# Kernel optimization log

Hardware: AMD Instinct MI355X
Metric: run time of the kernel (lower is better)

The kernel has to match this reference:

```python
import jax, jax.numpy as jnp
import numpy as np

N_NODES = 100000
N_EDGES = 1600000
IN_FEATS = 128
HEADS = 4
OUT_FEATS = 32
NEG_SLOPE = 0.2


def setup_inputs() -> dict:
    key = jax.random.key(0)
    k1, k2, k3, k4, k5, k6 = jax.random.split(key, 6)
    feat = jax.random.normal(k1, (N_NODES, IN_FEATS), dtype=jnp.float32)
    # nn.Linear(in_feats, out_feats*num_heads).weight -> [H*D_out, D_in]
    W = jax.random.normal(k2, (HEADS * OUT_FEATS, IN_FEATS), dtype=jnp.float32) * (1.0 / np.sqrt(IN_FEATS))
    attn_l = jax.random.normal(k3, (1, HEADS, OUT_FEATS), dtype=jnp.float32) * 0.1
    attn_r = jax.random.normal(k4, (1, HEADS, OUT_FEATS), dtype=jnp.float32) * 0.1
    src = jax.random.randint(k5, (N_EDGES,), 0, N_NODES, dtype=jnp.int32)
    dst = jax.random.randint(k6, (N_EDGES,), 0, N_NODES, dtype=jnp.int32)
    return {"feat": feat, "W": W, "attn_l": attn_l, "attn_r": attn_r, "src": src, "dst": dst}


def reference(feat, W, attn_l, attn_r, src, dst):
    N = feat.shape[0]
    H, D = attn_l.shape[1], attn_l.shape[2]
    # fc: feat @ W.T -> [N, H, D]
    ft = (feat @ W.T).reshape(N, H, D)
    el = jnp.sum(ft * attn_l, axis=-1)  # [N, H]
    er = jnp.sum(ft * attn_r, axis=-1)  # [N, H]
    # SDDMM edge scores (u_add_v) + leaky relu
    e = el[src] + er[dst]  # [E, H]
    e = jnp.where(e > 0, e, NEG_SLOPE * e)
    # segment softmax over edges grouped by destination node
    emax = jax.ops.segment_max(e, dst, num_segments=N)  # [N, H]
    ez = jnp.exp(e - emax[dst])
    esum = jax.ops.segment_sum(ez, dst, num_segments=N)  # [N, H]
    a = ez / esum[dst]  # [E, H]
    # weighted SpMM aggregation (u_mul_e + sum by dst)
    out = jax.ops.segment_sum(ft[src] * a[:, :, None], dst, num_segments=N)  # [N, H, D]
    return out
```

## Files before the change

### kernel.cpp

```cpp
#include <hip/hip_runtime.h>
#include <hip/hip_fp16.h>

#define IN_FEATS 128
#define HEADS 4
#define D_OUT 32
#define HD 128
#define NEG_SLOPE 0.2f

#define BSHIFT 8
#define BSIZE 256
#define CAP 4608

typedef _Float16 half8 __attribute__((ext_vector_type(8)));
typedef _Float16 half4v __attribute__((ext_vector_type(4)));
typedef float floatx4 __attribute__((ext_vector_type(4)));

#define LSTR 40
#define OSTR 136

__global__ __launch_bounds__(256) void gemm_ft(const float* __restrict__ feat,
                                               const float* __restrict__ W,
                                               const float* __restrict__ al,
                                               const float* __restrict__ ar,
                                               __half* __restrict__ ft_h,
                                               float* __restrict__ el,
                                               float* __restrict__ er,
                                               int* __restrict__ bcursor,
                                               int N, int NB) {
    __shared__ __align__(16) _Float16 sh[128 * OSTR];
    _Float16* Als = sh;
    _Float16* Wls = sh + 5120;
    const int t = threadIdx.x;
    const int w = t >> 6, lane = t & 63, quad = lane >> 4, l15 = lane & 15;
    const int nodeBase = blockIdx.x * 128;

    if (blockIdx.x == 0)
        for (int b = t; b < NB; b += 256) bcursor[b] = b * CAP;

    floatx4 acc[2][8] = {};

    for (int kk = 0; kk < 4; ++kk) {
        const int k0 = kk * 32;
#pragma unroll
        for (int i = 0; i < 4; ++i) {
            int idx = i * 256 + t;
            int row = idx >> 3;
            int q = idx & 7;
            int node = nodeBase + row;
            float4 v = make_float4(0.f, 0.f, 0.f, 0.f);
            if (node < N) v = *(const float4*)(feat + (size_t)node * IN_FEATS + k0 + q * 4);
            half4v hv = {(_Float16)v.x, (_Float16)v.y, (_Float16)v.z, (_Float16)v.w};
            *(half4v*)&Als[row * LSTR + q * 4] = hv;
            float4 wv = *(const float4*)(W + (size_t)row * IN_FEATS + k0 + q * 4);
            half4v hw = {(_Float16)wv.x, (_Float16)wv.y, (_Float16)wv.z, (_Float16)wv.w};
            *(half4v*)&Wls[row * LSTR + q * 4] = hw;
        }
        __syncthreads();
        half8 af0 = *(half8*)&Als[(w * 32 + l15) * LSTR + quad * 8];
        half8 af1 = *(half8*)&Als[(w * 32 + 16 + l15) * LSTR + quad * 8];
        half8 bf[8];
#pragma unroll
        for (int nt = 0; nt < 8; ++nt)
            bf[nt] = *(half8*)&Wls[(nt * 16 + l15) * LSTR + quad * 8];
#pragma unroll
        for (int nt = 0; nt < 8; ++nt) {
            acc[0][nt] = __builtin_amdgcn_mfma_f32_16x16x32_f16(af0, bf[nt], acc[0][nt], 0, 0, 0);
            acc[1][nt] = __builtin_amdgcn_mfma_f32_16x16x32_f16(af1, bf[nt], acc[1][nt], 0, 0, 0);
        }
        __syncthreads();
    }

#pragma unroll
    for (int mt = 0; mt < 2; ++mt)
#pragma unroll
        for (int nt = 0; nt < 8; ++nt)
#pragma unroll
            for (int r = 0; r < 4; ++r)
                sh[(w * 32 + mt * 16 + quad * 4 + r) * OSTR + nt * 16 + l15] =
                    (_Float16)acc[mt][nt][r];
    __syncthreads();

    const int row = t >> 1, seg = t & 1;
    const int node = nodeBase + row;
    half8 hv[8];
#pragma unroll
    for (int j = 0; j < 8; ++j) hv[j] = *(half8*)&sh[row * OSTR + seg * 64 + j * 8];

    float accl0 = 0.f, accl1 = 0.f, accr0 = 0.f, accr1 = 0.f;
#pragma unroll
    for (int j = 0; j < 8; ++j) {
        float4 a0 = *(const float4*)(al + seg * 64 + j * 8);
        float4 a1 = *(const float4*)(al + seg * 64 + j * 8 + 4);
        float4 r0 = *(const float4*)(ar + seg * 64 + j * 8);
        float4 r1 = *(const float4*)(ar + seg * 64 + j * 8 + 4);
        float v0 = (float)hv[j][0], v1 = (float)hv[j][1], v2 = (float)hv[j][2], v3 = (float)hv[j][3];
        float v4 = (float)hv[j][4], v5 = (float)hv[j][5], v6 = (float)hv[j][6], v7 = (float)hv[j][7];
        float dl = v0 * a0.x + v1 * a0.y + v2 * a0.z + v3 * a0.w
                 + v4 * a1.x + v5 * a1.y + v6 * a1.z + v7 * a1.w;
        float dr = v0 * r0.x + v1 * r0.y + v2 * r0.z + v3 * r0.w
                 + v4 * r1.x + v5 * r1.y + v6 * r1.z + v7 * r1.w;
        if (j < 4) { accl0 += dl; accr0 += dr; }
        else       { accl1 += dl; accr1 += dr; }
    }
    if (node < N) {
#pragma unroll
        for (int j = 0; j < 8; ++j)
            *(half8*)(ft_h + (size_t)node * HD + seg * 64 + j * 8) = hv[j];
        el[node * 4 + seg * 2 + 0] = accl0;
        el[node * 4 + seg * 2 + 1] = accl1;
        er[node * 4 + seg * 2 + 0] = accr0;
        er[node * 4 + seg * 2 + 1] = accr1;
    }
}

#define MAXCHUNK 3200

__global__ __launch_bounds__(256) void bin_scatter(const int* __restrict__ src,
                                                   const int* __restrict__ dst,
                                                   int* __restrict__ bcursor,
                                                   int* __restrict__ bedge,
                                                   int E, int NB, int chunk) {
    __shared__ int recL[MAXCHUNK];
    __shared__ unsigned short bL[MAXCHUNK];
    __shared__ int cnt[512];
    __shared__ int base[512];
    int t = threadIdx.x;
    int e0 = blockIdx.x * chunk;
    if (e0 >= E) return;
    int e1 = e0 + chunk; if (e1 > E) e1 = E;
    int ne = e1 - e0;
    cnt[t] = 0; cnt[t + 256] = 0;
    __syncthreads();
    for (int i = t; i < ne; i += 256) {
        int d = dst[e0 + i];
        int s = src[e0 + i];
        int b = d >> BSHIFT;
        recL[i] = s | ((d & (BSIZE - 1)) << 17);
        bL[i] = (unsigned short)b;
        atomicAdd(&cnt[b], 1);
    }
    __syncthreads();
    for (int b = t; b < NB; b += 256) {
        int c = cnt[b];
        base[b] = c ? atomicAdd(&bcursor[b], c) : 0;
    }
    __syncthreads();
    cnt[t] = 0; cnt[t + 256] = 0;
    __syncthreads();
    for (int i = t; i < ne; i += 256) {
        int b = bL[i];
        int p = base[b] + atomicAdd(&cnt[b], 1);
        if (p < (b + 1) * CAP)
            bedge[p] = recL[i];
    }
}

__global__ __launch_bounds__(256) void bucket_csr(const int* __restrict__ bcursor,
                                                  int* __restrict__ bedge,
                                                  int* __restrict__ row_start,
                                                  int* __restrict__ row_end, int N) {
    __shared__ int eL[CAP];
    __shared__ int cnt[256];
    __shared__ int sc[256];
    int b = blockIdx.x, t = threadIdx.x;
    int s0 = b * CAP;
    int cntE = bcursor[b] - s0;
    cnt[t] = 0;
    __syncthreads();
    for (int i = t; i < cntE; i += 256) {
        int v = bedge[s0 + i];
        eL[i] = v;
        atomicAdd(&cnt[v >> 17], 1);
    }
    __syncthreads();
    sc[t] = cnt[t];
    __syncthreads();
    for (int off = 1; off < 256; off <<= 1) {
        int v = (t >= off) ? sc[t - off] : 0;
        __syncthreads();
        sc[t] += v;
        __syncthreads();
    }
    int node0 = b << BSHIFT;
    int ex = sc[t] - cnt[t];
    if (node0 + t < N) {
        row_start[node0 + t] = s0 + ex;
        row_end[node0 + t] = s0 + sc[t];
    }
    __syncthreads();
    cnt[t] = ex;
    __syncthreads();
    for (int i = t; i < cntE; i += 256) {
        int v = eL[i];
        int p = atomicAdd(&cnt[v >> 17], 1);
        bedge[s0 + p] = v & 0x1FFFF;
    }
}

__global__ __launch_bounds__(256) void aggregate(const __half* __restrict__ ft_h,
                                                 const float* __restrict__ el,
                                                 const float* __restrict__ er,
                                                 const int* __restrict__ row_start,
                                                 const int* __restrict__ row_end,
                                                 const int* __restrict__ bedge,
                                                 float* __restrict__ out, int N) {
    int wid = threadIdx.x >> 6, lane = threadIdx.x & 63;
    int n = blockIdx.x * 4 + wid;
    if (n >= N) return;
    int start = row_start[n];
    int end = row_end[n];
    int g = lane >> 4;
    int q = lane & 15;
    int h = q >> 2;

    float er_h = er[(size_t)n * 4 + h];

    float a0 = 0.f, a1 = 0.f, a2 = 0.f, a3 = 0.f;
    float a4 = 0.f, a5 = 0.f, a6 = 0.f, a7 = 0.f;
    float ws = 0.f;
    for (int e = start + g; e < end; e += 4) {
        int s = bedge[e] & 0x1FFFF;
        float x = el[(size_t)s * 4 + h] + er_h;
        x = x > 0.f ? x : NEG_SLOPE * x;
        float w = __expf(x);
        int4 raw = *(const int4*)(ft_h + (size_t)s * HD + q * 8);
        float2 f0 = __half22float2(*(__half2*)&raw.x);
        float2 f1 = __half22float2(*(__half2*)&raw.y);
        float2 f2 = __half22float2(*(__half2*)&raw.z);
        float2 f3 = __half22float2(*(__half2*)&raw.w);
        a0 += w * f0.x; a1 += w * f0.y;
        a2 += w * f1.x; a3 += w * f1.y;
        a4 += w * f2.x; a5 += w * f2.y;
        a6 += w * f3.x; a7 += w * f3.y;
        ws += w;
    }
    a0 += __shfl_xor(a0, 16); a0 += __shfl_xor(a0, 32);
    a1 += __shfl_xor(a1, 16); a1 += __shfl_xor(a1, 32);
    a2 += __shfl_xor(a2, 16); a2 += __shfl_xor(a2, 32);
    a3 += __shfl_xor(a3, 16); a3 += __shfl_xor(a3, 32);
    a4 += __shfl_xor(a4, 16); a4 += __shfl_xor(a4, 32);
    a5 += __shfl_xor(a5, 16); a5 += __shfl_xor(a5, 32);
    a6 += __shfl_xor(a6, 16); a6 += __shfl_xor(a6, 32);
    a7 += __shfl_xor(a7, 16); a7 += __shfl_xor(a7, 32);
    ws += __shfl_xor(ws, 16); ws += __shfl_xor(ws, 32);
    float inv = ws > 0.f ? 1.0f / ws : 0.f;
    float r0 = (g == 0 ? a0 : g == 1 ? a2 : g == 2 ? a4 : a6) * inv;
    float r1 = (g == 0 ? a1 : g == 1 ? a3 : g == 2 ? a5 : a7) * inv;
    *(float2*)(out + (size_t)n * HD + q * 8 + g * 2) = make_float2(r0, r1);
}

extern "C" void kernel_launch(void* const* d_in, const int* in_sizes, int n_in,
                              void* d_out, int out_size, void* d_ws, size_t ws_size,
                              hipStream_t stream) {
    const float* feat = (const float*)d_in[0];
    const float* W    = (const float*)d_in[1];
    const float* al   = (const float*)d_in[2];
    const float* ar   = (const float*)d_in[3];
    const int* src    = (const int*)d_in[4];
    const int* dst    = (const int*)d_in[5];
    float* out        = (float*)d_out;

    const int N = in_sizes[0] / IN_FEATS;
    const int E = in_sizes[4];
    const int NB = (N + BSIZE - 1) >> BSHIFT;

    char* ws = (char*)d_ws;
    size_t off = 0;
    auto alloc = [&](size_t bytes) {
        void* p = ws + off;
        off += (bytes + 255) & ~(size_t)255;
        return p;
    };
    __half* ft_h     = (__half*)alloc((size_t)N * HD * 2);
    float* el        = (float*)alloc((size_t)N * 4 * 4);
    float* er        = (float*)alloc((size_t)N * 4 * 4);
    int*   row_start = (int*)alloc((size_t)N * 4);
    int*   row_end   = (int*)alloc((size_t)N * 4);
    int*   bcursor   = (int*)alloc(512 * 4);
    int*   bedge     = (int*)alloc((size_t)NB * CAP * 4);
    (void)ws_size;

    gemm_ft<<<(N + 127) / 128, 256, 0, stream>>>(feat, W, al, ar, ft_h, el, er, bcursor, N, NB);
    int grid2 = 512;
    int chunk = (E + grid2 - 1) / grid2;
    if (chunk > MAXCHUNK) chunk = MAXCHUNK;
    int nblk = (E + chunk - 1) / chunk;
    bin_scatter<<<nblk, 256, 0, stream>>>(src, dst, bcursor, bedge, E, NB, chunk);
    bucket_csr<<<NB, 256, 0, stream>>>(bcursor, bedge, row_start, row_end, N);
    aggregate<<<(N + 3) / 4, 256, 0, stream>>>(ft_h, el, er, row_start, row_end, bedge, out, N);
}
```

Baseline: 257.3 us.

## Fuse bucket CSR build into aggregation with smaller buckets and edge prefetch

```diff
diff --git a/kernel.cpp b/kernel.cpp
--- a/kernel.cpp
+++ b/kernel.cpp
@@ -7,9 +7,10 @@
 #define HD 128
 #define NEG_SLOPE 0.2f
 
-#define BSHIFT 8
-#define BSIZE 256
-#define CAP 4608
+#define BSHIFT 6
+#define BSIZE 64
+#define CAP 1280
+#define NBMAX 1600
 
 typedef _Float16 half8 __attribute__((ext_vector_type(8)));
 typedef _Float16 half4v __attribute__((ext_vector_type(4)));
@@ -122,14 +123,14 @@
                                                    int E, int NB, int chunk) {
     __shared__ int recL[MAXCHUNK];
     __shared__ unsigned short bL[MAXCHUNK];
-    __shared__ int cnt[512];
-    __shared__ int base[512];
+    __shared__ int cnt[NBMAX];
+    __shared__ int base[NBMAX];
     int t = threadIdx.x;
     int e0 = blockIdx.x * chunk;
     if (e0 >= E) return;
     int e1 = e0 + chunk; if (e1 > E) e1 = E;
     int ne = e1 - e0;
-    cnt[t] = 0; cnt[t + 256] = 0;
+    for (int b = t; b < NB; b += 256) cnt[b] = 0;
     __syncthreads();
     for (int i = t; i < ne; i += 256) {
         int d = dst[e0 + i];
@@ -145,7 +146,7 @@
         base[b] = c ? atomicAdd(&bcursor[b], c) : 0;
     }
     __syncthreads();
-    cnt[t] = 0; cnt[t + 256] = 0;
+    for (int b = t; b < NB; b += 256) cnt[b] = 0;
     __syncthreads();
     for (int i = t; i < ne; i += 256) {
         int b = bL[i];
@@ -155,98 +156,107 @@
     }
 }
 
-__global__ __launch_bounds__(256) void bucket_csr(const int* __restrict__ bcursor,
-                                                  int* __restrict__ bedge,
-                                                  int* __restrict__ row_start,
-                                                  int* __restrict__ row_end, int N) {
-    __shared__ int eL[CAP];
-    __shared__ int cnt[256];
-    __shared__ int sc[256];
-    int b = blockIdx.x, t = threadIdx.x;
-    int s0 = b * CAP;
+__global__ __launch_bounds__(256) void bucket_aggregate(const __half* __restrict__ ft_h,
+                                                        const float* __restrict__ el,
+                                                        const float* __restrict__ er,
+                                                        const int* __restrict__ bcursor,
+                                                        const int* __restrict__ bedge,
+                                                        float* __restrict__ out, int N) {
+    __shared__ int eRaw[CAP];
+    __shared__ int eS[CAP];
+    __shared__ int cnt[BSIZE];
+    __shared__ int exs[BSIZE];
+    __shared__ int pos[BSIZE];
+    const int b = blockIdx.x, t = threadIdx.x;
+    const int s0 = b * CAP;
     int cntE = bcursor[b] - s0;
-    cnt[t] = 0;
+    if (cntE > CAP) cntE = CAP;
+    if (t < BSIZE) cnt[t] = 0;
     __syncthreads();
     for (int i = t; i < cntE; i += 256) {
         int v = bedge[s0 + i];
-        eL[i] = v;
+        eRaw[i] = v;
         atomicAdd(&cnt[v >> 17], 1);
     }
     __syncthreads();
-    sc[t] = cnt[t];
-    __syncthreads();
-    for (int off = 1; off < 256; off <<= 1) {
-        int v = (t >= off) ? sc[t - off] : 0;
-        __syncthreads();
-        sc[t] += v;
-        __syncthreads();
-    }
-    int node0 = b << BSHIFT;
-    int ex = sc[t] - cnt[t];
-    if (node0 + t < N) {
-        row_start[node0 + t] = s0 + ex;
-        row_end[node0 + t] = s0 + sc[t];
-    }
-    __syncthreads();
-    cnt[t] = ex;
+    if (t < BSIZE) {
+        int x = cnt[t];
+        int inc = x;
+#pragma unroll
+        for (int off = 1; off < 64; off <<= 1) {
+            int y = __shfl_up(inc, off);
+            if (t >= off) inc += y;
+        }
+        exs[t] = inc - x;
+        pos[t] = inc - x;
+    }
     __syncthreads();
     for (int i = t; i < cntE; i += 256) {
-        int v = eL[i];
-        int p = atomicAdd(&cnt[v >> 17], 1);
-        bedge[s0 + p] = v & 0x1FFFF;
-    }
-}
-
-__global__ __launch_bounds__(256) void aggregate(const __half* __restrict__ ft_h,
-                                                 const float* __restrict__ el,
-                                                 const float* __restrict__ er,
-                                                 const int* __restrict__ row_start,
-                                                 const int* __restrict__ row_end,
-                                                 const int* __restrict__ bedge,
-                                                 float* __restrict__ out, int N) {
-    int wid = threadIdx.x >> 6, lane = threadIdx.x & 63;
-    int n = blockIdx.x * 4 + wid;
-    if (n >= N) return;
-    int start = row_start[n];
-    int end = row_end[n];
-    int g = lane >> 4;
-    int q = lane & 15;
-    int h = q >> 2;
-
-    float er_h = er[(size_t)n * 4 + h];
-
-    float a0 = 0.f, a1 = 0.f, a2 = 0.f, a3 = 0.f;
-    float a4 = 0.f, a5 = 0.f, a6 = 0.f, a7 = 0.f;
-    float ws = 0.f;
-    for (int e = start + g; e < end; e += 4) {
-        int s = bedge[e] & 0x1FFFF;
-        float x = el[(size_t)s * 4 + h] + er_h;
-        x = x > 0.f ? x : NEG_SLOPE * x;
-        float w = __expf(x);
-        int4 raw = *(const int4*)(ft_h + (size_t)s * HD + q * 8);
-        float2 f0 = __half22float2(*(__half2*)&raw.x);
-        float2 f1 = __half22float2(*(__half2*)&raw.y);
-        float2 f2 = __half22float2(*(__half2*)&raw.z);
-        float2 f3 = __half22float2(*(__half2*)&raw.w);
-        a0 += w * f0.x; a1 += w * f0.y;
-        a2 += w * f1.x; a3 += w * f1.y;
-        a4 += w * f2.x; a5 += w * f2.y;
-        a6 += w * f3.x; a7 += w * f3.y;
-        ws += w;
-    }
-    a0 += __shfl_xor(a0, 16); a0 += __shfl_xor(a0, 32);
-    a1 += __shfl_xor(a1, 16); a1 += __shfl_xor(a1, 32);
-    a2 += __shfl_xor(a2, 16); a2 += __shfl_xor(a2, 32);
-    a3 += __shfl_xor(a3, 16); a3 += __shfl_xor(a3, 32);
-    a4 += __shfl_xor(a4, 16); a4 += __shfl_xor(a4, 32);
-    a5 += __shfl_xor(a5, 16); a5 += __shfl_xor(a5, 32);
-    a6 += __shfl_xor(a6, 16); a6 += __shfl_xor(a6, 32);
-    a7 += __shfl_xor(a7, 16); a7 += __shfl_xor(a7, 32);
-    ws += __shfl_xor(ws, 16); ws += __shfl_xor(ws, 32);
-    float inv = ws > 0.f ? 1.0f / ws : 0.f;
-    float r0 = (g == 0 ? a0 : g == 1 ? a2 : g == 2 ? a4 : a6) * inv;
-    float r1 = (g == 0 ? a1 : g == 1 ? a3 : g == 2 ? a5 : a7) * inv;
-    *(float2*)(out + (size_t)n * HD + q * 8 + g * 2) = make_float2(r0, r1);
+        int v = eRaw[i];
+        int p = atomicAdd(&pos[v >> 17], 1);
+        eS[p] = v & 0x1FFFF;
+    }
+    __syncthreads();
+
+    const int wid = t >> 6, lane = t & 63;
+    const int g = lane >> 4;
+    const int q = lane & 15;
+    const int h = q >> 2;
+    const int node0 = b << BSHIFT;
+
+    for (int dl = wid; dl < BSIZE; dl += 4) {
+        int n = node0 + dl;
+        if (n >= N) break;
+        int start = exs[dl];
+        int end = start + cnt[dl];
+        float er_h = er[(size_t)n * 4 + h];
+
+        float a0 = 0.f, a1 = 0.f, a2 = 0.f, a3 = 0.f;
+        float a4 = 0.f, a5 = 0.f, a6 = 0.f, a7 = 0.f;
+        float ws = 0.f;
+
+        int e = start + g;
+        int s = (e < end) ? eS[e] : -1;
+        float elv = (s >= 0) ? el[(size_t)s * 4 + h] : 0.f;
+        int4 raw = make_int4(0, 0, 0, 0);
+        if (s >= 0) raw = *(const int4*)(ft_h + (size_t)s * HD + q * 8);
+
+        while (e < end) {
+            int en = e + 4;
+            int sn = (en < end) ? eS[en] : -1;
+            float eln = (sn >= 0) ? el[(size_t)sn * 4 + h] : 0.f;
+            int4 rawn = make_int4(0, 0, 0, 0);
+            if (sn >= 0) rawn = *(const int4*)(ft_h + (size_t)sn * HD + q * 8);
+
+            float x = elv + er_h;
+            x = x > 0.f ? x : NEG_SLOPE * x;
+            float w = __expf(x);
+            float2 f0 = __half22float2(*(__half2*)&raw.x);
+            float2 f1 = __half22float2(*(__half2*)&raw.y);
+            float2 f2 = __half22float2(*(__half2*)&raw.z);
+            float2 f3 = __half22float2(*(__half2*)&raw.w);
+            a0 += w * f0.x; a1 += w * f0.y;
+            a2 += w * f1.x; a3 += w * f1.y;
+            a4 += w * f2.x; a5 += w * f2.y;
+            a6 += w * f3.x; a7 += w * f3.y;
+            ws += w;
+
+            e = en; s = sn; elv = eln; raw = rawn;
+        }
+        a0 += __shfl_xor(a0, 16); a0 += __shfl_xor(a0, 32);
+        a1 += __shfl_xor(a1, 16); a1 += __shfl_xor(a1, 32);
+        a2 += __shfl_xor(a2, 16); a2 += __shfl_xor(a2, 32);
+        a3 += __shfl_xor(a3, 16); a3 += __shfl_xor(a3, 32);
+        a4 += __shfl_xor(a4, 16); a4 += __shfl_xor(a4, 32);
+        a5 += __shfl_xor(a5, 16); a5 += __shfl_xor(a5, 32);
+        a6 += __shfl_xor(a6, 16); a6 += __shfl_xor(a6, 32);
+        a7 += __shfl_xor(a7, 16); a7 += __shfl_xor(a7, 32);
+        ws += __shfl_xor(ws, 16); ws += __shfl_xor(ws, 32);
+        float inv = ws > 0.f ? 1.0f / ws : 0.f;
+        float r0 = (g == 0 ? a0 : g == 1 ? a2 : g == 2 ? a4 : a6) * inv;
+        float r1 = (g == 0 ? a1 : g == 1 ? a3 : g == 2 ? a5 : a7) * inv;
+        *(float2*)(out + (size_t)n * HD + q * 8 + g * 2) = make_float2(r0, r1);
+    }
 }
 
 extern "C" void kernel_launch(void* const* d_in, const int* in_sizes, int n_in,
@@ -271,13 +281,11 @@
         off += (bytes + 255) & ~(size_t)255;
         return p;
     };
-    __half* ft_h     = (__half*)alloc((size_t)N * HD * 2);
-    float* el        = (float*)alloc((size_t)N * 4 * 4);
-    float* er        = (float*)alloc((size_t)N * 4 * 4);
-    int*   row_start = (int*)alloc((size_t)N * 4);
-    int*   row_end   = (int*)alloc((size_t)N * 4);
-    int*   bcursor   = (int*)alloc(512 * 4);
-    int*   bedge     = (int*)alloc((size_t)NB * CAP * 4);
+    __half* ft_h   = (__half*)alloc((size_t)N * HD * 2);
+    float* el      = (float*)alloc((size_t)N * 4 * 4);
+    float* er      = (float*)alloc((size_t)N * 4 * 4);
+    int*   bcursor = (int*)alloc((size_t)NBMAX * 4);
+    int*   bedge   = (int*)alloc((size_t)NB * CAP * 4);
     (void)ws_size;
 
     gemm_ft<<<(N + 127) / 128, 256, 0, stream>>>(feat, W, al, ar, ft_h, el, er, bcursor, N, NB);
@@ -286,6 +294,5 @@
     if (chunk > MAXCHUNK) chunk = MAXCHUNK;
     int nblk = (E + chunk - 1) / chunk;
     bin_scatter<<<nblk, 256, 0, stream>>>(src, dst, bcursor, bedge, E, NB, chunk);
-    bucket_csr<<<NB, 256, 0, stream>>>(bcursor, bedge, row_start, row_end, N);
-    aggregate<<<(N + 3) / 4, 256, 0, stream>>>(ft_h, el, er, row_start, row_end, bedge, out, N);
-}
+    bucket_aggregate<<<NB, 256, 0, stream>>>(ft_h, el, er, bcursor, bedge, out, N);
+}
```

After: 252.4 us. Within noise of the previous version (-1.9%).
